# Performance work log

Measured on AMD Instinct MI355X. Metric: run time of the kernel, lower is better.

Reference implementation:

```python
import jax, jax.numpy as jnp
import numpy as np

K = 3  # Chebyshev order (number of coefficients)


def setup_inputs() -> dict:
    key = jax.random.key(0)
    k1, k2, k3, k4 = jax.random.split(key, 4)
    B, nNode, c_in, T = 16, 512, 32, 64
    c_out = 64
    x = jax.random.normal(k1, (B, nNode, c_in, T), dtype=jnp.float32)
    # scaled Laplacian-like batched adjacency; scale keeps the Chebyshev
    # recursion numerically tame (spectral norm ~ O(1))
    adj = jax.random.normal(k2, (B, nNode, nNode), dtype=jnp.float32) * (1.0 / np.sqrt(nNode))
    # 1x1 conv params: weight [c_out, K*c_in], bias [c_out]
    W = jax.random.normal(k3, (c_out, K * c_in), dtype=jnp.float32) * 0.1
    b = jax.random.normal(k4, (c_out,), dtype=jnp.float32) * 0.1
    return {"x": x, "adj": adj, "W": W, "b": b}


def reference(x, adj, W, b):
    # x: [B, nNode, c_in, T] -> permute(0,2,1,3) -> [B, c_in, nNode, T]
    x = jnp.transpose(x, (0, 2, 1, 3))
    B, c_in, nNode, T = x.shape
    # Chebyshev recursion: L0 = I, L1 = adj, L_k = 2*adj@L_{k-1} - L_{k-2}
    L0 = jnp.broadcast_to(jnp.eye(nNode, dtype=x.dtype), (B, nNode, nNode))
    L1 = adj
    Ls = [L0, L1]
    for _ in range(2, K):
        L2 = 2.0 * jnp.matmul(adj, L1) - L0
        L0, L1 = L1, L2
        Ls.append(L2)
    Lap = jnp.stack(Ls, axis=1)              # [B, K, nNode, nNode]
    Lap = jnp.swapaxes(Lap, -1, -2)          # transpose(-1, -2)
    # einsum 'bcnl,bknq->bckql' then view [B, c_in*K, nNode, T]
    y = jnp.einsum('bcnl,bknq->bckql', x, Lap)  # [B, c_in, K, nNode, T]
    y = y.reshape(B, c_in * K, nNode, T)
    # 1x1 Conv2d: channel mixing + bias
    out = jnp.einsum('oc,bcnl->bonl', W, y) + b[None, :, None, None]
    return out
```

## Files before the change

### kernel.cpp

```cpp
#include <hip/hip_runtime.h>

typedef unsigned short u16;
typedef __bf16 v8bf __attribute__((ext_vector_type(8)));
typedef float f32x4 __attribute__((ext_vector_type(4)));
typedef u16 us8 __attribute__((ext_vector_type(8)));
typedef u16 us4 __attribute__((ext_vector_type(4)));

static __device__ __forceinline__ u16 f2bf(float f) {
  union { __bf16 h; u16 u; } cv;
  cv.h = (__bf16)f;
  return cv.u;
}

static __device__ __forceinline__ void gl_lds16(const u16* g, u16* l) {
  __builtin_amdgcn_global_load_lds(
      (const __attribute__((address_space(1))) unsigned int*)g,
      (__attribute__((address_space(3))) unsigned int*)l, 16, 0, 0);
}

__global__ __launch_bounds__(256)
void prep_k(const float* __restrict__ adj, u16* __restrict__ adj_bf,
            u16* __restrict__ adjT_bf, const float* __restrict__ x,
            u16* __restrict__ xT, const float* __restrict__ W,
            u16* __restrict__ Mb) {
  const int bid = blockIdx.x;
  const int tid = threadIdx.x;
  __shared__ u16 Ls[64][68];
  if (bid < 1024) {
    const int b = bid >> 6;
    const int r0 = ((bid >> 3) & 7) * 64;
    const int c0 = (bid & 7) * 64;
#pragma unroll
    for (int i = 0; i < 4; ++i) {
      const int idx = tid + 256 * i;
      const int r = idx >> 4;
      const int c4 = (idx & 15) * 4;
      const float4 v = *(const float4*)(adj + ((size_t)(b * 512 + r0 + r) * 512 + c0 + c4));
      us4 o;
      o[0] = f2bf(v.x); o[1] = f2bf(v.y); o[2] = f2bf(v.z); o[3] = f2bf(v.w);
      *(us4*)&Ls[r][c4] = o;
      *(us4*)(adj_bf + ((size_t)(b * 512 + r0 + r) * 512 + c0 + c4)) = o;
    }
    __syncthreads();
#pragma unroll
    for (int i = 0; i < 2; ++i) {
      const int idx = tid + 256 * i;
      const int c = idx >> 3;
      const int r8 = (idx & 7) * 8;
      us8 o;
#pragma unroll
      for (int j = 0; j < 8; ++j) o[j] = Ls[r8 + j][c];
      *(us8*)(adjT_bf + ((size_t)(b * 512 + c0 + c) * 512 + r0 + r8)) = o;
    }
  } else if (bid < 5120) {
    const int t = bid - 1024;
    const int b = t >> 8;
    const int q0 = ((t >> 5) & 7) * 64;
    const int j0 = (t & 31) * 64;
#pragma unroll
    for (int i = 0; i < 4; ++i) {
      const int idx = tid + 256 * i;
      const int r = idx >> 4;
      const int j4 = (idx & 15) * 4;
      const float4 v = *(const float4*)(x + ((size_t)(b * 512 + q0 + r) * 2048 + j0 + j4));
      us4 o;
      o[0] = f2bf(v.x); o[1] = f2bf(v.y); o[2] = f2bf(v.z); o[3] = f2bf(v.w);
      *(us4*)&Ls[r][j4] = o;
    }
    __syncthreads();
#pragma unroll
    for (int i = 0; i < 2; ++i) {
      const int idx = tid + 256 * i;
      const int jp = idx >> 3;
      const int q8 = (idx & 7) * 8;
      us8 o;
#pragma unroll
      for (int j = 0; j < 8; ++j) o[j] = Ls[q8 + j][jp];
      *(us8*)(xT + ((size_t)(b * 2048 + j0 + jp) * 512 + q0 + q8)) = o;
    }
  } else {
    for (int i = tid; i < 64 * 96; i += 256) {
      const int cc = i % 96;
      const int r = cc % 3;
      const float w = W[i];
      const float m = (r == 0) ? (w - W[i + 2]) : w;
      Mb[i] = f2bf(m);
    }
  }
}

__global__ __launch_bounds__(256)
void gemm_sq(const u16* __restrict__ A, const u16* __restrict__ BT,
             u16* __restrict__ C) {
  const int b = blockIdx.z;
  const int row0 = blockIdx.y * 128;
  const int col0 = blockIdx.x * 128;
  const u16* Ab = A + (size_t)b * 512 * 512;
  const u16* BTb = BT + (size_t)b * 512 * 512;

  __shared__ u16 smem[16384];
  u16* As = smem;
  u16* Bs = smem + 8192;

  const int tid = threadIdx.x;
  const int lane = tid & 63;
  const int w = tid >> 6;
  const int wm = (w >> 1) * 64;
  const int wn = (w & 1) * 64;
  const int l16 = lane & 15;
  const int kg = lane >> 4;

  f32x4 acc[4][4];
#pragma unroll
  for (int m = 0; m < 4; ++m)
#pragma unroll
    for (int n = 0; n < 4; ++n) acc[m][n] = (f32x4){0.f, 0.f, 0.f, 0.f};

  for (int k0 = 0; k0 < 512; k0 += 64) {
    __syncthreads();
#pragma unroll
    for (int i = 0; i < 4; ++i) {
      const int eb = w * 2048 + i * 512;
      const int e = eb + lane * 8;
      const int r = e >> 6;
      const int kk = e & 63;
      gl_lds16(Ab + (size_t)(row0 + r) * 512 + k0 + kk, As + eb);
      gl_lds16(BTb + (size_t)(col0 + r) * 512 + k0 + kk, Bs + eb);
    }
    __syncthreads();
#pragma unroll
    for (int ks = 0; ks < 2; ++ks) {
      v8bf af[4], bfr[4];
#pragma unroll
      for (int m = 0; m < 4; ++m)
        af[m] = *(const v8bf*)(As + (wm + m * 16 + l16) * 64 + ks * 32 + kg * 8);
#pragma unroll
      for (int n = 0; n < 4; ++n)
        bfr[n] = *(const v8bf*)(Bs + (wn + n * 16 + l16) * 64 + ks * 32 + kg * 8);
#pragma unroll
      for (int m = 0; m < 4; ++m)
#pragma unroll
        for (int n = 0; n < 4; ++n)
          acc[m][n] = __builtin_amdgcn_mfma_f32_16x16x32_bf16(af[m], bfr[n], acc[m][n], 0, 0, 0);
    }
  }
  u16* Cb = C + (size_t)b * 512 * 512;
#pragma unroll
  for (int m = 0; m < 4; ++m)
#pragma unroll
    for (int n = 0; n < 4; ++n)
#pragma unroll
      for (int v = 0; v < 4; ++v) {
        const int rr = row0 + wm + m * 16 + kg * 4 + v;
        const int cc = col0 + wn + n * 16 + l16;
        Cb[(size_t)rr * 512 + cc] = f2bf(2.0f * acc[m][n][v]);
      }
}

__global__ __launch_bounds__(512, 4)
void prop_k(const u16* __restrict__ A1, const u16* __restrict__ A2,
            const u16* __restrict__ BT, u16* __restrict__ X1,
            u16* __restrict__ Y2) {
  const int fid = blockIdx.x + 16 * (blockIdx.y + 4 * blockIdx.z);
  const int wk = (fid & 7) * 128 + (fid >> 3);
  const int b = wk >> 6;
  const int row0 = ((wk >> 4) & 3) * 128;
  const int col0 = (wk & 15) * 128;

  const u16* A1b = A1 + (size_t)b * 512 * 512;
  const u16* A2b = A2 + (size_t)b * 512 * 512;
  const u16* BTb = BT + (size_t)b * 2048 * 512;

  __shared__ u16 smem[2][3][4096];

  const int tid = threadIdx.x;
  const int lane = tid & 63;
  const int w = tid >> 6;
  const int wq = w & 3;
  const int wm = (wq >> 1) * 64;
  const int wn = (wq & 1) * 64;
  const int l16 = lane & 15;
  const int kg = lane >> 4;

  const int sc = w * 64 + lane;
  const int skg = sc >> 7;
  const int srow = sc & 127;
  const int sdst = sc * 8;
  const size_t sA = (size_t)(row0 + srow) * 512 + skg * 8;
  const size_t sB = (size_t)(col0 + srow) * 512 + skg * 8;

  f32x4 acc[4][4];
#pragma unroll
  for (int m = 0; m < 4; ++m)
#pragma unroll
    for (int n = 0; n < 4; ++n) acc[m][n] = (f32x4){0.f, 0.f, 0.f, 0.f};

  gl_lds16(A1b + sA, &smem[0][0][sdst]);
  gl_lds16(A2b + sA, &smem[0][1][sdst]);
  gl_lds16(BTb + sB, &smem[0][2][sdst]);
  __syncthreads();

  for (int t = 0; t < 16; ++t) {
    const int cur = t & 1;
    if (t < 15) {
      const int k0 = (t + 1) * 32;
      gl_lds16(A1b + sA + k0, &smem[cur ^ 1][0][sdst]);
      gl_lds16(A2b + sA + k0, &smem[cur ^ 1][1][sdst]);
      gl_lds16(BTb + sB + k0, &smem[cur ^ 1][2][sdst]);
    }
    const u16* As = (w < 4) ? smem[cur][0] : smem[cur][1];
    const u16* Bs = smem[cur][2];
    v8bf af[4], bfr[4];
#pragma unroll
    for (int m = 0; m < 4; ++m)
      af[m] = *(const v8bf*)(As + (kg * 128 + wm + m * 16 + l16) * 8);
#pragma unroll
    for (int n = 0; n < 4; ++n)
      bfr[n] = *(const v8bf*)(Bs + (kg * 128 + wn + n * 16 + l16) * 8);
    __builtin_amdgcn_s_setprio(1);
#pragma unroll
    for (int m = 0; m < 4; ++m)
#pragma unroll
      for (int n = 0; n < 4; ++n)
        acc[m][n] = __builtin_amdgcn_mfma_f32_16x16x32_bf16(af[m], bfr[n], acc[m][n], 0, 0, 0);
    __builtin_amdgcn_s_setprio(0);
    __syncthreads();
  }

  u16* Db = ((w < 4) ? X1 : Y2) + (size_t)b * 512 * 2048;
#pragma unroll
  for (int m = 0; m < 4; ++m)
#pragma unroll
    for (int n = 0; n < 4; ++n)
#pragma unroll
      for (int v = 0; v < 4; ++v) {
        const int rr = row0 + wm + m * 16 + kg * 4 + v;
        const int cc = col0 + wn + n * 16 + l16;
        Db[(size_t)rr * 2048 + cc] = f2bf(acc[m][n][v]);
      }
}

__global__ __launch_bounds__(256)
void mix_mfma(const float* __restrict__ x0, const u16* __restrict__ x1,
              const u16* __restrict__ y2, const u16* __restrict__ Mb,
              const float* __restrict__ bias, float* __restrict__ out) {
  const int q = blockIdx.x;
  const int b = blockIdx.y;
  __shared__ u16 Vt[64][104];
  __shared__ u16 Ms[64][104];
  const int tid = threadIdx.x;
  const int lane = tid & 63;
  const int w = tid >> 6;
  const int l16 = lane & 15;
  const int kg = lane >> 4;

#pragma unroll
  for (int i = 0; i < 3; ++i) {
    const int idx = tid + 256 * i;
    const int o = idx / 12;
    const int c8 = (idx % 12) * 8;
    *(uint4*)&Ms[o][c8] = *(const uint4*)(Mb + o * 96 + c8);
  }
  const size_t base = ((size_t)b * 512 + q) * 2048;
#pragma unroll
  for (int i = 0; i < 2; ++i) {
    const int idx = tid + 256 * i;
    const int c = idx >> 4;
    const int l0 = (idx & 15) * 4;
    const float4 v = *(const float4*)(x0 + base + c * 64 + l0);
    Vt[l0 + 0][3 * c] = f2bf(v.x);
    Vt[l0 + 1][3 * c] = f2bf(v.y);
    Vt[l0 + 2][3 * c] = f2bf(v.z);
    Vt[l0 + 3][3 * c] = f2bf(v.w);
  }
  {
    const int c = tid >> 3;
    const int l0 = (tid & 7) * 8;
    const us8 v1 = *(const us8*)(x1 + base + c * 64 + l0);
    const us8 v2 = *(const us8*)(y2 + base + c * 64 + l0);
#pragma unroll
    for (int j = 0; j < 8; ++j) {
      Vt[l0 + j][3 * c + 1] = v1[j];
      Vt[l0 + j][3 * c + 2] = v2[j];
    }
  }
  __syncthreads();

  f32x4 acc[4];
#pragma unroll
  for (int n = 0; n < 4; ++n) acc[n] = (f32x4){0.f, 0.f, 0.f, 0.f};
#pragma unroll
  for (int ks = 0; ks < 3; ++ks) {
    const v8bf a = *(const v8bf*)&Ms[w * 16 + l16][ks * 32 + kg * 8];
#pragma unroll
    for (int n = 0; n < 4; ++n) {
      const v8bf bv = *(const v8bf*)&Vt[n * 16 + l16][ks * 32 + kg * 8];
      acc[n] = __builtin_amdgcn_mfma_f32_16x16x32_bf16(a, bv, acc[n], 0, 0, 0);
    }
  }
#pragma unroll
  for (int n = 0; n < 4; ++n)
#pragma unroll
    for (int v = 0; v < 4; ++v) {
      const int o = w * 16 + kg * 4 + v;
      out[(((size_t)b * 64 + o) * 512 + q) * 64 + n * 16 + l16] = acc[n][v] + bias[o];
    }
}

extern "C" void kernel_launch(void* const* d_in, const int* in_sizes, int n_in,
                              void* d_out, int out_size, void* d_ws, size_t ws_size,
                              hipStream_t stream) {
  const float* x   = (const float*)d_in[0];
  const float* adj = (const float*)d_in[1];
  const float* W   = (const float*)d_in[2];
  const float* bia = (const float*)d_in[3];
  float* out = (float*)d_out;

  u16* adj_bf  = (u16*)d_ws;
  u16* adjT_bf = adj_bf  + (size_t)16 * 512 * 512;
  u16* adj2_bf = adjT_bf + (size_t)16 * 512 * 512;
  u16* xT      = adj2_bf + (size_t)16 * 512 * 512;
  u16* X1      = xT      + (size_t)16 * 2048 * 512;
  u16* Y2      = X1      + (size_t)16 * 512 * 2048;
  u16* Mb      = Y2      + (size_t)16 * 512 * 2048;

  hipLaunchKernelGGL(prep_k, dim3(5121), dim3(256), 0, stream,
                     adj, adj_bf, adjT_bf, x, xT, W, Mb);
  hipLaunchKernelGGL(gemm_sq, dim3(4, 4, 16), dim3(256), 0, stream,
                     adj_bf, adjT_bf, adj2_bf);
  hipLaunchKernelGGL(prop_k, dim3(16, 4, 16), dim3(512), 0, stream,
                     adj_bf, adj2_bf, xT, X1, Y2);
  hipLaunchKernelGGL(mix_mfma, dim3(512, 16), dim3(256), 0, stream,
                     x, X1, Y2, Mb, bia, out);
}
```

Baseline: 161.9 us.

## Stack adj and adj2 into one operand and run prop as plain tiled GEMM

Stores adj and 2·adj² contiguously per batch as a 1024x512 matrix, so the propagation step becomes one GEMM of 1024x512 by 512x2048. It writes X1 and Y2 into a single stacked buffer. The dual-A 512-thread prop kernel, which shared each B tile between two A operands and double-buffered 32-wide K steps with direct-to-LDS loads, is replaced by a 256-thread 128x128 tile kernel. That kernel uses 64-wide K steps with a single buffer and two barriers per step. This simplifies the kernel and doubles the grid, but loses the B-tile sharing across the two A operands and the load/compute overlap.

```diff
diff --git a/kernel.cpp b/kernel.cpp
--- a/kernel.cpp
+++ b/kernel.cpp
@@ -19,7 +19,7 @@
 }
 
 __global__ __launch_bounds__(256)
-void prep_k(const float* __restrict__ adj, u16* __restrict__ adj_bf,
+void prep_k(const float* __restrict__ adj, u16* __restrict__ adjC,
             u16* __restrict__ adjT_bf, const float* __restrict__ x,
             u16* __restrict__ xT, const float* __restrict__ W,
             u16* __restrict__ Mb) {
@@ -39,7 +39,7 @@
       us4 o;
       o[0] = f2bf(v.x); o[1] = f2bf(v.y); o[2] = f2bf(v.z); o[3] = f2bf(v.w);
       *(us4*)&Ls[r][c4] = o;
-      *(us4*)(adj_bf + ((size_t)(b * 512 + r0 + r) * 512 + c0 + c4)) = o;
+      *(us4*)(adjC + ((size_t)(b * 1024 + r0 + r) * 512 + c0 + c4)) = o;
     }
     __syncthreads();
 #pragma unroll
@@ -90,12 +90,12 @@
 }
 
 __global__ __launch_bounds__(256)
-void gemm_sq(const u16* __restrict__ A, const u16* __restrict__ BT,
-             u16* __restrict__ C) {
+void gemm_sq(const u16* __restrict__ adjC_in, const u16* __restrict__ BT,
+             u16* __restrict__ adjC) {
   const int b = blockIdx.z;
   const int row0 = blockIdx.y * 128;
   const int col0 = blockIdx.x * 128;
-  const u16* Ab = A + (size_t)b * 512 * 512;
+  const u16* Ab = adjC_in + (size_t)b * 1024 * 512;
   const u16* BTb = BT + (size_t)b * 512 * 512;
 
   __shared__ u16 smem[16384];
@@ -144,7 +144,7 @@
           acc[m][n] = __builtin_amdgcn_mfma_f32_16x16x32_bf16(af[m], bfr[n], acc[m][n], 0, 0, 0);
     }
   }
-  u16* Cb = C + (size_t)b * 512 * 512;
+  u16* Cb = adjC + (size_t)b * 1024 * 512 + (size_t)512 * 512;
 #pragma unroll
   for (int m = 0; m < 4; ++m)
 #pragma unroll
@@ -157,77 +157,64 @@
       }
 }
 
-__global__ __launch_bounds__(512, 4)
-void prop_k(const u16* __restrict__ A1, const u16* __restrict__ A2,
-            const u16* __restrict__ BT, u16* __restrict__ X1,
-            u16* __restrict__ Y2) {
-  const int fid = blockIdx.x + 16 * (blockIdx.y + 4 * blockIdx.z);
-  const int wk = (fid & 7) * 128 + (fid >> 3);
-  const int b = wk >> 6;
-  const int row0 = ((wk >> 4) & 3) * 128;
+__global__ __launch_bounds__(256)
+void prop_k(const u16* __restrict__ AC, const u16* __restrict__ BT,
+            u16* __restrict__ C) {
+  const int fid = blockIdx.x + 16 * (blockIdx.y + 8 * blockIdx.z);
+  const int wk = (fid & 7) * 256 + (fid >> 3);
+  const int b = wk >> 7;
+  const int row0 = ((wk >> 4) & 7) * 128;
   const int col0 = (wk & 15) * 128;
-
-  const u16* A1b = A1 + (size_t)b * 512 * 512;
-  const u16* A2b = A2 + (size_t)b * 512 * 512;
+  const u16* Ab = AC + (size_t)b * 1024 * 512;
   const u16* BTb = BT + (size_t)b * 2048 * 512;
 
-  __shared__ u16 smem[2][3][4096];
+  __shared__ u16 smem[16384];
+  u16* As = smem;
+  u16* Bs = smem + 8192;
 
   const int tid = threadIdx.x;
   const int lane = tid & 63;
   const int w = tid >> 6;
-  const int wq = w & 3;
-  const int wm = (wq >> 1) * 64;
-  const int wn = (wq & 1) * 64;
+  const int wm = (w >> 1) * 64;
+  const int wn = (w & 1) * 64;
   const int l16 = lane & 15;
   const int kg = lane >> 4;
 
-  const int sc = w * 64 + lane;
-  const int skg = sc >> 7;
-  const int srow = sc & 127;
-  const int sdst = sc * 8;
-  const size_t sA = (size_t)(row0 + srow) * 512 + skg * 8;
-  const size_t sB = (size_t)(col0 + srow) * 512 + skg * 8;
-
   f32x4 acc[4][4];
 #pragma unroll
   for (int m = 0; m < 4; ++m)
 #pragma unroll
     for (int n = 0; n < 4; ++n) acc[m][n] = (f32x4){0.f, 0.f, 0.f, 0.f};
 
-  gl_lds16(A1b + sA, &smem[0][0][sdst]);
-  gl_lds16(A2b + sA, &smem[0][1][sdst]);
-  gl_lds16(BTb + sB, &smem[0][2][sdst]);
-  __syncthreads();
-
-  for (int t = 0; t < 16; ++t) {
-    const int cur = t & 1;
-    if (t < 15) {
-      const int k0 = (t + 1) * 32;
-      gl_lds16(A1b + sA + k0, &smem[cur ^ 1][0][sdst]);
-      gl_lds16(A2b + sA + k0, &smem[cur ^ 1][1][sdst]);
-      gl_lds16(BTb + sB + k0, &smem[cur ^ 1][2][sdst]);
-    }
-    const u16* As = (w < 4) ? smem[cur][0] : smem[cur][1];
-    const u16* Bs = smem[cur][2];
-    v8bf af[4], bfr[4];
-#pragma unroll
-    for (int m = 0; m < 4; ++m)
-      af[m] = *(const v8bf*)(As + (kg * 128 + wm + m * 16 + l16) * 8);
-#pragma unroll
-    for (int n = 0; n < 4; ++n)
-      bfr[n] = *(const v8bf*)(Bs + (kg * 128 + wn + n * 16 + l16) * 8);
-    __builtin_amdgcn_s_setprio(1);
-#pragma unroll
-    for (int m = 0; m < 4; ++m)
+  for (int k0 = 0; k0 < 512; k0 += 64) {
+    __syncthreads();
+#pragma unroll
+    for (int i = 0; i < 4; ++i) {
+      const int eb = w * 2048 + i * 512;
+      const int e = eb + lane * 8;
+      const int r = e >> 6;
+      const int kk = e & 63;
+      gl_lds16(Ab + (size_t)(row0 + r) * 512 + k0 + kk, As + eb);
+      gl_lds16(BTb + (size_t)(col0 + r) * 512 + k0 + kk, Bs + eb);
+    }
+    __syncthreads();
+#pragma unroll
+    for (int ks = 0; ks < 2; ++ks) {
+      v8bf af[4], bfr[4];
+#pragma unroll
+      for (int m = 0; m < 4; ++m)
+        af[m] = *(const v8bf*)(As + (wm + m * 16 + l16) * 64 + ks * 32 + kg * 8);
 #pragma unroll
       for (int n = 0; n < 4; ++n)
-        acc[m][n] = __builtin_amdgcn_mfma_f32_16x16x32_bf16(af[m], bfr[n], acc[m][n], 0, 0, 0);
-    __builtin_amdgcn_s_setprio(0);
-    __syncthreads();
-  }
-
-  u16* Db = ((w < 4) ? X1 : Y2) + (size_t)b * 512 * 2048;
+        bfr[n] = *(const v8bf*)(Bs + (wn + n * 16 + l16) * 64 + ks * 32 + kg * 8);
+#pragma unroll
+      for (int m = 0; m < 4; ++m)
+#pragma unroll
+        for (int n = 0; n < 4; ++n)
+          acc[m][n] = __builtin_amdgcn_mfma_f32_16x16x32_bf16(af[m], bfr[n], acc[m][n], 0, 0, 0);
+    }
+  }
+  u16* Cb = C + (size_t)b * 1024 * 2048;
 #pragma unroll
   for (int m = 0; m < 4; ++m)
 #pragma unroll
@@ -236,14 +223,14 @@
       for (int v = 0; v < 4; ++v) {
         const int rr = row0 + wm + m * 16 + kg * 4 + v;
         const int cc = col0 + wn + n * 16 + l16;
-        Db[(size_t)rr * 2048 + cc] = f2bf(acc[m][n][v]);
+        Cb[(size_t)rr * 2048 + cc] = f2bf(acc[m][n][v]);
       }
 }
 
 __global__ __launch_bounds__(256)
-void mix_mfma(const float* __restrict__ x0, const u16* __restrict__ x1,
-              const u16* __restrict__ y2, const u16* __restrict__ Mb,
-              const float* __restrict__ bias, float* __restrict__ out) {
+void mix_mfma(const float* __restrict__ x0, const u16* __restrict__ X1Y2,
+              const u16* __restrict__ Mb, const float* __restrict__ bias,
+              float* __restrict__ out) {
   const int q = blockIdx.x;
   const int b = blockIdx.y;
   __shared__ u16 Vt[64][104];
@@ -261,13 +248,15 @@
     const int c8 = (idx % 12) * 8;
     *(uint4*)&Ms[o][c8] = *(const uint4*)(Mb + o * 96 + c8);
   }
-  const size_t base = ((size_t)b * 512 + q) * 2048;
+  const size_t base0 = ((size_t)b * 512 + q) * 2048;
+  const size_t base1 = ((size_t)b * 1024 + q) * 2048;
+  const size_t base2 = ((size_t)b * 1024 + 512 + q) * 2048;
 #pragma unroll
   for (int i = 0; i < 2; ++i) {
     const int idx = tid + 256 * i;
     const int c = idx >> 4;
     const int l0 = (idx & 15) * 4;
-    const float4 v = *(const float4*)(x0 + base + c * 64 + l0);
+    const float4 v = *(const float4*)(x0 + base0 + c * 64 + l0);
     Vt[l0 + 0][3 * c] = f2bf(v.x);
     Vt[l0 + 1][3 * c] = f2bf(v.y);
     Vt[l0 + 2][3 * c] = f2bf(v.z);
@@ -276,8 +265,8 @@
   {
     const int c = tid >> 3;
     const int l0 = (tid & 7) * 8;
-    const us8 v1 = *(const us8*)(x1 + base + c * 64 + l0);
-    const us8 v2 = *(const us8*)(y2 + base + c * 64 + l0);
+    const us8 v1 = *(const us8*)(X1Y2 + base1 + c * 64 + l0);
+    const us8 v2 = *(const us8*)(X1Y2 + base2 + c * 64 + l0);
 #pragma unroll
     for (int j = 0; j < 8; ++j) {
       Vt[l0 + j][3 * c + 1] = v1[j];
@@ -316,20 +305,18 @@
   const float* bia = (const float*)d_in[3];
   float* out = (float*)d_out;
 
-  u16* adj_bf  = (u16*)d_ws;
-  u16* adjT_bf = adj_bf  + (size_t)16 * 512 * 512;
-  u16* adj2_bf = adjT_bf + (size_t)16 * 512 * 512;
-  u16* xT      = adj2_bf + (size_t)16 * 512 * 512;
-  u16* X1      = xT      + (size_t)16 * 2048 * 512;
-  u16* Y2      = X1      + (size_t)16 * 512 * 2048;
-  u16* Mb      = Y2      + (size_t)16 * 512 * 2048;
+  u16* adjC    = (u16*)d_ws;
+  u16* adjT_bf = adjC    + (size_t)16 * 1024 * 512;
+  u16* xT      = adjT_bf + (size_t)16 * 512 * 512;
+  u16* X1Y2    = xT      + (size_t)16 * 2048 * 512;
+  u16* Mb      = X1Y2    + (size_t)16 * 1024 * 2048;
 
   hipLaunchKernelGGL(prep_k, dim3(5121), dim3(256), 0, stream,
-                     adj, adj_bf, adjT_bf, x, xT, W, Mb);
+                     adj, adjC, adjT_bf, x, xT, W, Mb);
   hipLaunchKernelGGL(gemm_sq, dim3(4, 4, 16), dim3(256), 0, stream,
-                     adj_bf, adjT_bf, adj2_bf);
-  hipLaunchKernelGGL(prop_k, dim3(16, 4, 16), dim3(512), 0, stream,
-                     adj_bf, adj2_bf, xT, X1, Y2);
+                     adjC, adjT_bf, adjC);
+  hipLaunchKernelGGL(prop_k, dim3(16, 8, 16), dim3(256), 0, stream,
+                     adjC, xT, X1Y2);
   hipLaunchKernelGGL(mix_mfma, dim3(512, 16), dim3(256), 0, stream,
-                     x, X1, Y2, Mb, bia, out);
-}
+                     x, X1Y2, Mb, bia, out);
+}
```

After: 154.4 us. 4.6% less time.
